# Optimization experiments

Hardware: AMD Instinct MI355X
Metric: run time of the kernel (lower is better)

## Reference

```python
import jax, jax.numpy as jnp
import numpy as np

B, L, D = 4, 2048, 2048
H, KVH = 16, 4
HD = D // H            # 128
G = H // KVH           # GQA group size
K_SEL = L // 4         # top_k_ratio = 0.25 -> 512
MAX_SEQ = 8192
THETA = 10000.0
SCALE = HD ** -0.5
NEG = -1e9


def _rope_tables(dim, max_len, theta):
    inv = 1.0 / theta ** (jnp.arange(0, dim, 2, dtype=jnp.float32) / dim)  # (dim/2,)
    ang = jnp.arange(max_len, dtype=jnp.float32)[:, None] * inv[None, :]   # (max_len, dim/2)
    return jnp.cos(ang), jnp.sin(ang)


def _apply_rope_pos(x, cos, sin, pos):
    # x: (B, h, K, HD), pos: (B, K) int positions
    c = cos[pos][:, None]  # (B,1,K,HD/2)
    s = sin[pos][:, None]
    x1, x2 = jnp.split(x, 2, axis=-1)
    return jnp.concatenate([x1 * c - x2 * s, x1 * s + x2 * c], axis=-1)


def setup_inputs() -> dict:
    key = jax.random.key(0)
    ks = jax.random.split(key, 8)
    std = 0.02
    x   = jax.random.normal(ks[0], (B, L, D), dtype=jnp.float32)
    Wq  = jax.random.normal(ks[1], (D, D), dtype=jnp.float32) * std
    Wkv = jax.random.normal(ks[2], (D, 2 * KVH * HD), dtype=jnp.float32) * std
    Wo  = jax.random.normal(ks[3], (D, D), dtype=jnp.float32) * std
    W1  = jax.random.normal(ks[4], (D, D // 4), dtype=jnp.float32) * std
    b1  = jnp.zeros((D // 4,), dtype=jnp.float32)
    W2  = jax.random.normal(ks[5], (D // 4, 1), dtype=jnp.float32) * std
    b2  = jnp.zeros((1,), dtype=jnp.float32)
    return {"x": x, "Wq": Wq, "Wkv": Wkv, "Wo": Wo,
            "W1": W1, "b1": b1, "W2": W2, "b2": b2}


def reference(x, Wq, Wkv, Wo, W1, b1, W2, b2):
    Bx, Lx, Dx = x.shape
    # 1. learned per-token importance scores
    imp = (jax.nn.gelu(x @ W1 + b1, approximate=False) @ W2 + b2)[..., 0]  # (B,L)
    # 2. top-k token selection, sorted to keep original order
    _, idx = jax.lax.top_k(imp, K_SEL)
    idx = jnp.sort(idx, axis=-1)                                           # (B,K)
    x_sel = jnp.take_along_axis(x, idx[..., None], axis=1)                 # (B,K,D)
    # 3. fused KV projection on the selected subset (GQA)
    kv = x_sel @ Wkv
    k, v = jnp.split(kv, 2, axis=-1)
    k = k.reshape(Bx, K_SEL, KVH, HD).transpose(0, 2, 1, 3)                # (B,KVH,K,HD)
    v = v.reshape(Bx, K_SEL, KVH, HD).transpose(0, 2, 1, 3)
    # 4. RoPE with original positions for K, contiguous positions for Q
    cos, sin = _rope_tables(HD, MAX_SEQ, THETA)
    k = _apply_rope_pos(k, cos, sin, idx)
    q = (x @ Wq).reshape(Bx, Lx, H, HD).transpose(0, 2, 1, 3)              # (B,H,L,HD)
    qpos = jnp.broadcast_to(jnp.arange(Lx)[None, :], (Bx, Lx))
    q = _apply_rope_pos(q, cos, sin, qpos)
    # 5. GQA head expansion + attention over gathered keys
    k = jnp.repeat(k, G, axis=1)                                           # (B,H,K,HD)
    v = jnp.repeat(v, G, axis=1)
    scores = jnp.einsum('bhld,bhkd->bhlk', q, k) * SCALE                   # (B,H,L,K)
    # causal mask on original key positions
    causal = idx[:, None, None, :] > jnp.arange(Lx)[None, None, :, None]
    scores = jnp.where(causal, NEG, scores)
    attn = jax.nn.softmax(scores, axis=-1)
    # 6. importance soft gating (gradient path into the scorer)
    gate = jax.nn.sigmoid(jnp.take_along_axis(imp, idx, axis=1))           # (B,K)
    attn = attn * gate[:, None, None, :]
    out = jnp.einsum('bhlk,bhkd->bhld', attn, v)                           # (B,H,L,HD)
    out = out.transpose(0, 2, 1, 3).reshape(Bx, Lx, Dx)
    return out @ Wo
```

## Files before the change

### kernel.cpp

```cpp
#include <hip/hip_runtime.h>
#include <math.h>

typedef unsigned short u16;
typedef __attribute__((ext_vector_type(8))) short short8;
typedef __attribute__((ext_vector_type(4))) float f32x4;

__device__ __forceinline__ float bf2f(u16 u) {
  return __uint_as_float(((unsigned)u) << 16);
}
__device__ __forceinline__ u16 f2bf(float f) {
  unsigned u = __float_as_uint(f);
  return (u16)((u + 0x7fffu + ((u >> 16) & 1u)) >> 16);
}

__device__ __forceinline__ void gload_lds16(const u16* g, u16* l) {
  __builtin_amdgcn_global_load_lds((const __attribute__((address_space(1))) unsigned int*)g,
                                   (__attribute__((address_space(3))) unsigned int*)l, 16, 0, 0);
}

__device__ __forceinline__ void stage_tile(const u16* __restrict__ gbase, int ldg,
                                           u16* lds, int w, int lane) {
  #pragma unroll
  for (int i = 0; i < 4; ++i) {
    int c = w * 4 + i;
    const u16* g = gbase + (size_t)(c * 8 + (lane >> 3)) * ldg + (lane & 7) * 8;
    gload_lds16(g, lds + c * 512);
  }
}

__global__ __launch_bounds__(256) void cvt_x_kernel(const float* __restrict__ x,
                                                    u16* __restrict__ xb,
                                                    u16* __restrict__ xlo) {
  size_t base = ((size_t)blockIdx.x * 256 + threadIdx.x) * 8;
  short8 hi, lo;
  #pragma unroll
  for (int i = 0; i < 8; ++i) {
    float v = x[base + i];
    u16 h = f2bf(v);
    hi[i] = (short)h;
    lo[i] = (short)f2bf(v - bf2f(h));
  }
  *(short8*)&xb[base] = hi;
  *(short8*)&xlo[base] = lo;
}

template <bool HILO>
__global__ __launch_bounds__(256) void transpose_cvt(const float* __restrict__ in,
                                                     u16* __restrict__ outH,
                                                     u16* __restrict__ outL,
                                                     int R, int C) {
  __shared__ u16 tH[64][72];
  __shared__ u16 tL[64][72];
  int rb = blockIdx.y * 64, cb = blockIdx.x * 64;
  int t = threadIdx.x;
  #pragma unroll
  for (int i = 0; i < 16; ++i) {
    int r = i * 4 + (t >> 6), c = t & 63;
    float v = in[(size_t)(rb + r) * C + cb + c];
    u16 h = f2bf(v);
    tH[r][c] = h;
    if (HILO) tL[r][c] = f2bf(v - bf2f(h));
  }
  __syncthreads();
  #pragma unroll
  for (int i = 0; i < 16; ++i) {
    int r = i * 4 + (t >> 6), c = t & 63;
    outH[(size_t)(cb + r) * R + rb + c] = tH[c][r];
    if (HILO) outL[(size_t)(cb + r) * R + rb + c] = tL[c][r];
  }
}

__global__ void ropetab_kernel(float* __restrict__ cosT, float* __restrict__ sinT) {
  int pos = blockIdx.x, i = threadIdx.x;
  float e = (float)(2 * i) * (1.0f / 128.0f);
  float inv = powf(10000.0f, -e);
  float ang = (float)pos * inv;
  cosT[pos * 64 + i] = cosf(ang);
  sinT[pos * 64 + i] = sinf(ang);
}

template <bool BF16OUT>
__global__ __launch_bounds__(512, 2) void gemm256(const u16* __restrict__ A,
                                                  const u16* __restrict__ BT,
                                                  float* __restrict__ Cf,
                                                  u16* __restrict__ Cb,
                                                  int M, int N, int K) {
  __shared__ __align__(1024) u16 smem[65536];
  const int bm = blockIdx.x * 256, bn = blockIdx.y * 256;
  const int t = threadIdx.x, lane = t & 63, w = t >> 6;
  const int ll = lane & 15, lh = lane >> 4;
  const int wr = w >> 2, wc = w & 3;
  const int NT = K >> 6;

  const int tt0 = t, tt1 = t + 512;
  const int r0 = tt0 >> 2, r1 = tt1 >> 2;
  const int c0 = (((tt0 & 3) ^ ((tt0 >> 3) & 3)) << 3);
  const int c1 = (((tt1 & 3) ^ ((tt1 >> 3) & 3)) << 3);
  const size_t aoff0 = (size_t)(bm + r0) * K + c0;
  const size_t aoff1 = (size_t)(bm + r1) * K + c1;
  const size_t boff0 = (size_t)(bn + r0) * K + c0;
  const size_t boff1 = (size_t)(bn + r1) * K + c1;

  const int swz = ((lh ^ ((ll >> 1) & 3)) << 3);
  const int arow = (wr * 128 + ll) * 32 + swz;
  const int brow = (wc * 64 + ll) * 32 + swz;

  f32x4 acc[8][4];
  #pragma unroll
  for (int mi = 0; mi < 8; ++mi)
    #pragma unroll
    for (int ni = 0; ni < 4; ++ni) acc[mi][ni] = f32x4{0.f, 0.f, 0.f, 0.f};

  short8 aq[8], bq[2];

#define G_STAGE(base, o0, o1, lds) \
  gload_lds16((base) + (o0), (lds) + w * 512); \
  gload_lds16((base) + (o1), (lds) + 4096 + w * 512)
#define RD_A(Sa, ks) \
  _Pragma("unroll") for (int mi = 0; mi < 8; ++mi) aq[mi] = *(const short8*)&(Sa)[(ks)*8192 + arow + mi * 512]
#define RD_B(Sb, ks, nh) \
  _Pragma("unroll") for (int n2 = 0; n2 < 2; ++n2) bq[n2] = *(const short8*)&(Sb)[(ks)*8192 + brow + ((nh)*2 + n2) * 512]
#define DO_MFMA(nh) \
  __builtin_amdgcn_s_setprio(1); \
  _Pragma("unroll") for (int mi = 0; mi < 8; ++mi) \
    _Pragma("unroll") for (int n2 = 0; n2 < 2; ++n2) \
      acc[mi][(nh)*2 + n2] = __builtin_amdgcn_mfma_f32_16x16x32_bf16(aq[mi], bq[n2], acc[mi][(nh)*2 + n2], 0, 0, 0); \
  __builtin_amdgcn_s_setprio(0)
#define VMW(n) asm volatile("s_waitcnt vmcnt(" #n ")" ::: "memory")

  G_STAGE(A, aoff0, aoff1, smem);
  G_STAGE(BT, boff0, boff1, smem + 16384);
  G_STAGE(A, aoff0 + 32, aoff1 + 32, smem + 8192);
  G_STAGE(BT, boff0 + 32, boff1 + 32, smem + 16384 + 8192);

  for (int kt = 0; kt < NT - 1; ++kt) {
    const int cur = kt & 1;
    u16* Sa = smem + cur * 32768;
    u16* Sb = Sa + 16384;
    u16* Pa = smem + (cur ^ 1) * 32768;
    u16* Pb = Pa + 16384;
    const size_t kg = (size_t)(kt + 1) * 64;
    VMW(4);
    __builtin_amdgcn_s_barrier();
    G_STAGE(A, aoff0 + kg, aoff1 + kg, Pa);
    RD_A(Sa, 0);
    RD_B(Sb, 0, 0);
    DO_MFMA(0);
    __builtin_amdgcn_s_barrier();
    G_STAGE(BT, boff0 + kg, boff1 + kg, Pb);
    RD_B(Sb, 0, 1);
    DO_MFMA(1);
    VMW(4);
    __builtin_amdgcn_s_barrier();
    G_STAGE(A, aoff0 + kg + 32, aoff1 + kg + 32, Pa + 8192);
    RD_A(Sa, 1);
    RD_B(Sb, 1, 0);
    DO_MFMA(0);
    __builtin_amdgcn_s_barrier();
    G_STAGE(BT, boff0 + kg + 32, boff1 + kg + 32, Pb + 8192);
    RD_B(Sb, 1, 1);
    DO_MFMA(1);
  }
  {
    const int cur = (NT - 1) & 1;
    u16* Sa = smem + cur * 32768;
    u16* Sb = Sa + 16384;
    VMW(4);
    __builtin_amdgcn_s_barrier();
    RD_A(Sa, 0); RD_B(Sb, 0, 0); DO_MFMA(0);
    __builtin_amdgcn_s_barrier();
    RD_B(Sb, 0, 1); DO_MFMA(1);
    VMW(0);
    __builtin_amdgcn_s_barrier();
    RD_A(Sa, 1); RD_B(Sb, 1, 0); DO_MFMA(0);
    __builtin_amdgcn_s_barrier();
    RD_B(Sb, 1, 1); DO_MFMA(1);
  }

  #pragma unroll
  for (int mi = 0; mi < 8; ++mi)
    #pragma unroll
    for (int ni = 0; ni < 4; ++ni)
      #pragma unroll
      for (int r = 0; r < 4; ++r) {
        int row = bm + wr * 128 + mi * 16 + lh * 4 + r;
        int col = bn + wc * 64 + ni * 16 + ll;
        float v = acc[mi][ni][r];
        if (BF16OUT) Cb[(size_t)row * N + col] = f2bf(v);
        else Cf[(size_t)row * N + col] = v;
      }
#undef G_STAGE
#undef RD_A
#undef RD_B
#undef DO_MFMA
#undef VMW
}

__global__ __launch_bounds__(256) void gemm_bt_gather(const u16* __restrict__ A,
                                                      const u16* __restrict__ BT,
                                                      const int* __restrict__ rowidx,
                                                      float* __restrict__ Cpart,
                                                      int M, int N, int K) {
  constexpr int BK = 64;
  __shared__ u16 As[128][BK + 8];
  __shared__ u16 Bs[128][BK + 8];
  const int bm = blockIdx.x * 128, bn = blockIdx.y * 128;
  const int kz = blockIdx.z;
  const int t = threadIdx.x, lane = t & 63, w = t >> 6;
  const int lh = lane >> 4, ll = lane & 15;
  const int wm = (w >> 1) * 64, wn = (w & 1) * 64;
  f32x4 acc[4][4];
  #pragma unroll
  for (int mt = 0; mt < 4; ++mt)
    #pragma unroll
    for (int nt = 0; nt < 4; ++nt) acc[mt][nt] = f32x4{0.f, 0.f, 0.f, 0.f};

  const int k0 = kz * (K / 2), k1 = k0 + K / 2;
  for (int kb = k0; kb < k1; kb += BK) {
    __syncthreads();
    #pragma unroll
    for (int i = 0; i < 4; ++i) {
      int e = t + i * 256;
      int row = e >> 3, c8 = e & 7;
      int arow = rowidx[bm + row];
      *(short8*)&As[row][c8 * 8] = *(const short8*)&A[(size_t)arow * K + kb + c8 * 8];
      *(short8*)&Bs[row][c8 * 8] = *(const short8*)&BT[(size_t)(bn + row) * K + kb + c8 * 8];
    }
    __syncthreads();
    #pragma unroll
    for (int ks = 0; ks < 2; ++ks) {
      short8 a[4], b[4];
      #pragma unroll
      for (int mt = 0; mt < 4; ++mt) a[mt] = *(const short8*)&As[wm + mt * 16 + ll][ks * 32 + lh * 8];
      #pragma unroll
      for (int nt = 0; nt < 4; ++nt) b[nt] = *(const short8*)&Bs[wn + nt * 16 + ll][ks * 32 + lh * 8];
      #pragma unroll
      for (int mt = 0; mt < 4; ++mt)
        #pragma unroll
        for (int nt = 0; nt < 4; ++nt)
          acc[mt][nt] = __builtin_amdgcn_mfma_f32_16x16x32_bf16(a[mt], b[nt], acc[mt][nt], 0, 0, 0);
    }
  }
  float* C = Cpart + (size_t)kz * M * N;
  #pragma unroll
  for (int mt = 0; mt < 4; ++mt)
    #pragma unroll
    for (int nt = 0; nt < 4; ++nt)
      #pragma unroll
      for (int r = 0; r < 4; ++r) {
        int row = bm + wm + mt * 16 + lh * 4 + r;
        int col = bn + wn + nt * 16 + ll;
        C[(size_t)row * N + col] = acc[mt][nt][r];
      }
}

__global__ __launch_bounds__(512) void gemm_scorer(const u16* __restrict__ Ahi,
                                                   const u16* __restrict__ Alo,
                                                   const u16* __restrict__ Bhi,
                                                   const u16* __restrict__ Blo,
                                                   float* __restrict__ Cpart,
                                                   int M, int N, int K) {
  __shared__ __align__(1024) u16 smem[49152];
  const int bm = blockIdx.x * 256, bn = blockIdx.y * 128;
  const int kz = blockIdx.z;
  const int t = threadIdx.x, lane = t & 63, w = t >> 6;
  const int ll = lane & 15, lh = lane >> 4;
  const int wr = w >> 2, wc = w & 3;

  const int cA0 = (w * 2) * 64 + lane;
  const int cA1 = (w * 2 + 1) * 64 + lane;
  const int cB = w * 64 + lane;
  const size_t offA0 = (size_t)(bm + (cA0 >> 2)) * K + (((cA0 & 3) ^ ((cA0 >> 3) & 3)) << 3);
  const size_t offA1 = (size_t)(bm + (cA1 >> 2)) * K + (((cA1 & 3) ^ ((cA1 >> 3) & 3)) << 3);
  const size_t offB = (size_t)(bn + (cB >> 2)) * K + (((cB & 3) ^ ((cB >> 3) & 3)) << 3);

  const int arow = wr * 128 + ll;
  const int brow = wc * 32 + ll;

  f32x4 acc[8][2];
  #pragma unroll
  for (int mi = 0; mi < 8; ++mi)
    #pragma unroll
    for (int ni = 0; ni < 2; ++ni) acc[mi][ni] = f32x4{0.f, 0.f, 0.f, 0.f};

#define S_STAGE(buf, kb) \
  gload_lds16(Ahi + offA0 + (kb), (buf) + cA0 * 8); \
  gload_lds16(Ahi + offA1 + (kb), (buf) + cA1 * 8); \
  gload_lds16(Alo + offA0 + (kb), (buf) + 8192 + cA0 * 8); \
  gload_lds16(Alo + offA1 + (kb), (buf) + 8192 + cA1 * 8); \
  gload_lds16(Bhi + offB + (kb), (buf) + 16384 + cB * 8); \
  gload_lds16(Blo + offB + (kb), (buf) + 20480 + cB * 8)
#define SVMW(n) asm volatile("s_waitcnt vmcnt(" #n ")" ::: "memory")

  const int k0 = kz * (K / 2);
  const int NT = (K / 2) / 32;

  S_STAGE(smem, k0);

  for (int kt = 0; kt < NT; ++kt) {
    const int cur = kt & 1;
    u16* S = smem + cur * 24576;
    SVMW(0);
    __builtin_amdgcn_s_barrier();
    if (kt + 1 < NT) { S_STAGE(smem + (cur ^ 1) * 24576, k0 + (kt + 1) * 32); }

    short8 aH[8], aL[8], bH[2], bL[2];
    #pragma unroll
    for (int mi = 0; mi < 8; ++mi) {
      int r = arow + mi * 16;
      int o = r * 32 + ((lh ^ ((r >> 1) & 3)) << 3);
      aH[mi] = *(const short8*)&S[o];
      aL[mi] = *(const short8*)&S[8192 + o];
    }
    #pragma unroll
    for (int ni = 0; ni < 2; ++ni) {
      int r = brow + ni * 16;
      int o = r * 32 + ((lh ^ ((r >> 1) & 3)) << 3);
      bH[ni] = *(const short8*)&S[16384 + o];
      bL[ni] = *(const short8*)&S[20480 + o];
    }
    __builtin_amdgcn_s_setprio(1);
    #pragma unroll
    for (int mi = 0; mi < 8; ++mi)
      #pragma unroll
      for (int ni = 0; ni < 2; ++ni)
        acc[mi][ni] = __builtin_amdgcn_mfma_f32_16x16x32_bf16(aH[mi], bH[ni], acc[mi][ni], 0, 0, 0);
    __builtin_amdgcn_s_setprio(0);
    __builtin_amdgcn_s_setprio(1);
    #pragma unroll
    for (int mi = 0; mi < 8; ++mi)
      #pragma unroll
      for (int ni = 0; ni < 2; ++ni)
        acc[mi][ni] = __builtin_amdgcn_mfma_f32_16x16x32_bf16(aH[mi], bL[ni], acc[mi][ni], 0, 0, 0);
    __builtin_amdgcn_s_setprio(0);
    __builtin_amdgcn_s_setprio(1);
    #pragma unroll
    for (int mi = 0; mi < 8; ++mi)
      #pragma unroll
      for (int ni = 0; ni < 2; ++ni)
        acc[mi][ni] = __builtin_amdgcn_mfma_f32_16x16x32_bf16(aL[mi], bH[ni], acc[mi][ni], 0, 0, 0);
    __builtin_amdgcn_s_setprio(0);
    __builtin_amdgcn_s_barrier();
  }

  float* C = Cpart + (size_t)kz * M * N;
  #pragma unroll
  for (int mi = 0; mi < 8; ++mi)
    #pragma unroll
    for (int ni = 0; ni < 2; ++ni)
      #pragma unroll
      for (int r = 0; r < 4; ++r) {
        int row = bm + wr * 128 + mi * 16 + lh * 4 + r;
        int col = bn + wc * 32 + ni * 16 + ll;
        C[(size_t)row * N + col] = acc[mi][ni][r];
      }
#undef S_STAGE
#undef SVMW
}

__global__ __launch_bounds__(256) void scorer_finish(const float* __restrict__ hg,
                                                     const float* __restrict__ b1,
                                                     const float* __restrict__ W2,
                                                     const float* __restrict__ b2,
                                                     float* __restrict__ imp) {
  int tok = blockIdx.x * 4 + (threadIdx.x >> 6);
  int lane = threadIdx.x & 63;
  const float* h0 = hg + (size_t)tok * 512;
  const float* h1 = hg + (size_t)8192 * 512 + (size_t)tok * 512;
  float s = 0.f;
  #pragma unroll
  for (int i = 0; i < 8; ++i) {
    int c = lane + i * 64;
    float v = h0[c] + h1[c] + b1[c];
    v = 0.5f * v * (1.0f + erff(v * 0.70710678118654752f));
    s += v * W2[c];
  }
  #pragma unroll
  for (int off = 32; off; off >>= 1) s += __shfl_xor(s, off, 64);
  if (lane == 0) imp[tok] = s + b2[0];
}

__global__ __launch_bounds__(1024) void topk_kernel(const float* __restrict__ imp,
                                                    int* __restrict__ idx_sel,
                                                    int* __restrict__ sel_rows,
                                                    float* __restrict__ gatev) {
  __shared__ float v[2048];
  __shared__ int ix[2048];
  __shared__ int ids[512];
  int b = blockIdx.x, t = threadIdx.x;
  for (int i = t; i < 2048; i += 1024) { v[i] = imp[b * 2048 + i]; ix[i] = i; }
  __syncthreads();
  for (int k = 2; k <= 2048; k <<= 1)
    for (int j = k >> 1; j > 0; j >>= 1) {
      int i = ((t & ~(j - 1)) << 1) | (t & (j - 1));
      int l2 = i | j;
      bool dir = ((i & k) == 0);
      float vi = v[i], vl = v[l2];
      int xi = ix[i], xl = ix[l2];
      bool g = (vi < vl) || (vi == vl && xi > xl);
      if (g == dir) { v[i] = vl; v[l2] = vi; ix[i] = xl; ix[l2] = xi; }
      __syncthreads();
    }
  if (t < 512) ids[t] = ix[t];
  __syncthreads();
  for (int k = 2; k <= 512; k <<= 1)
    for (int j = k >> 1; j > 0; j >>= 1) {
      if (t < 256) {
        int i = ((t & ~(j - 1)) << 1) | (t & (j - 1));
        int l2 = i | j;
        bool dir = ((i & k) == 0);
        int ai = ids[i], al = ids[l2];
        if ((ai > al) == dir) { ids[i] = al; ids[l2] = ai; }
      }
      __syncthreads();
    }
  if (t < 512) {
    int id = ids[t];
    idx_sel[b * 512 + t] = id;
    sel_rows[b * 512 + t] = b * 2048 + id;
    float g = imp[b * 2048 + id];
    gatev[b * 512 + t] = 1.0f / (1.0f + __expf(-g));
  }
}

__global__ __launch_bounds__(256) void rope_k2(const float* __restrict__ part,
                                               const int* __restrict__ idx_sel,
                                               const float* __restrict__ cosT,
                                               const float* __restrict__ sinT,
                                               u16* __restrict__ Kb) {
  int gid = blockIdx.x * 256 + threadIdx.x;
  int i = gid & 63;
  int s = (gid >> 6) & 511;
  int kvh = (gid >> 15) & 3;
  int b = gid >> 17;
  size_t src = (size_t)(b * 512 + s) * 1024 + kvh * 128 + i;
  float k1 = part[src] + part[src + 2097152];
  float k2 = part[src + 64] + part[src + 64 + 2097152];
  int pos = idx_sel[b * 512 + s];
  float c = cosT[pos * 64 + i], sn = sinT[pos * 64 + i];
  size_t dst = (size_t)((b * 4 + kvh) * 512 + s) * 128 + i;
  Kb[dst] = f2bf(k1 * c - k2 * sn);
  Kb[dst + 64] = f2bf(k1 * sn + k2 * c);
}

__global__ __launch_bounds__(256) void vtrans2(const float* __restrict__ part,
                                               const float* __restrict__ gatev,
                                               u16* __restrict__ VT) {
  int gid = blockIdx.x * 256 + threadIdx.x;
  int s = gid & 511;
  int d = (gid >> 9) & 127;
  int kvh = (gid >> 16) & 3;
  int b = gid >> 18;
  size_t src = (size_t)(b * 512 + s) * 1024 + 512 + kvh * 128 + d;
  float v = part[src] + part[src + 2097152];
  VT[(size_t)((b * 4 + kvh) * 128 + d) * 512 + s] = f2bf(v * gatev[b * 512 + s]);
}

__global__ __launch_bounds__(512) void attn_kernel(const u16* __restrict__ Qb,
                                                   const u16* __restrict__ Kb,
                                                   const u16* __restrict__ VTb,
                                                   const int* __restrict__ idxp,
                                                   const float* __restrict__ cosT,
                                                   const float* __restrict__ sinT,
                                                   u16* __restrict__ Ob) {
  __shared__ u16 Ks[64][132];
  __shared__ u16 Vs[128][76];
  __shared__ u16 Ps[8][16][68];
  __shared__ int idx_s[64];

  const int qt = (blockIdx.x + 4 * blockIdx.z) & 15;
  const int h = blockIdx.y, b = blockIdx.z;
  const int kvh = h >> 2;
  const int t = threadIdx.x, lane = t & 63, w = t >> 6;
  const int lh = lane >> 4, ll = lane & 15;
  const int q0 = qt * 128;
  const float SCALE_LOG2E = 0.12753102331f;

  int NT = 8;
  if (idxp[b * 512] <= q0) {
    NT = 1;
    while (NT < 8 && idxp[b * 512 + NT * 64] <= q0 + 127) ++NT;
  }

  const int lrow = q0 + w * 16 + ll;
  short8 aq[4];
  #pragma unroll
  for (int ks = 0; ks < 4; ++ks)
    aq[ks] = *(const short8*)&Qb[(size_t)(b * 2048 + lrow) * 2048 + h * 128 + ks * 32 + lh * 8];
  {
    const float* cp = cosT + (size_t)lrow * 64 + lh * 8;
    const float* sp = sinT + (size_t)lrow * 64 + lh * 8;
    short8 n0, n1, n2, n3;
    #pragma unroll
    for (int j = 0; j < 8; ++j) {
      float cA = cp[j], sA = sp[j], cB = cp[32 + j], sB = sp[32 + j];
      float x0 = bf2f((u16)aq[0][j]), x2 = bf2f((u16)aq[2][j]);
      float x1 = bf2f((u16)aq[1][j]), x3 = bf2f((u16)aq[3][j]);
      n0[j] = (short)f2bf(x0 * cA - x2 * sA);
      n2[j] = (short)f2bf(x0 * sA + x2 * cA);
      n1[j] = (short)f2bf(x1 * cB - x3 * sB);
      n3[j] = (short)f2bf(x1 * sB + x3 * cB);
    }
    aq[0] = n0; aq[1] = n1; aq[2] = n2; aq[3] = n3;
  }

  float m[4], lden[4];
  f32x4 O[8];
  #pragma unroll
  for (int r = 0; r < 4; ++r) { m[r] = -INFINITY; lden[r] = 0.f; }
  #pragma unroll
  for (int dt = 0; dt < 8; ++dt) O[dt] = f32x4{0.f, 0.f, 0.f, 0.f};

  for (int kt = 0; kt < NT; ++kt) {
    const int tmax = idxp[b * 512 + kt * 64 + 63];
    const bool nomask = (tmax <= q0 + w * 16);

    __syncthreads();
    #pragma unroll
    for (int i = 0; i < 2; ++i) {
      int e = t + i * 512;
      int krow = e >> 4, kc8 = e & 15;
      *(short8*)&Ks[krow][kc8 * 8] =
          *(const short8*)&Kb[(size_t)((b * 4 + kvh) * 512 + kt * 64 + krow) * 128 + kc8 * 8];
      int vrow = e >> 3, vc8 = e & 7;
      *(short8*)&Vs[vrow][vc8 * 8] =
          *(const short8*)&VTb[(size_t)((b * 4 + kvh) * 128 + vrow) * 512 + kt * 64 + vc8 * 8];
    }
    if (t < 64) idx_s[t] = idxp[b * 512 + kt * 64 + t];
    __syncthreads();

    f32x4 S[4];
    #pragma unroll
    for (int nt = 0; nt < 4; ++nt) S[nt] = f32x4{0.f, 0.f, 0.f, 0.f};
    #pragma unroll
    for (int nt = 0; nt < 4; ++nt)
      #pragma unroll
      for (int ks = 0; ks < 4; ++ks) {
        short8 bk = *(const short8*)&Ks[nt * 16 + ll][ks * 32 + lh * 8];
        S[nt] = __builtin_amdgcn_mfma_f32_16x16x32_bf16(aq[ks], bk, S[nt], 0, 0, 0);
      }

    float p[4][4], lmax[4];
    #pragma unroll
    for (int r = 0; r < 4; ++r) lmax[r] = -INFINITY;
    if (nomask) {
      #pragma unroll
      for (int nt = 0; nt < 4; ++nt)
        #pragma unroll
        for (int r = 0; r < 4; ++r) {
          float s = S[nt][r] * SCALE_LOG2E;
          p[nt][r] = s;
          lmax[r] = fmaxf(lmax[r], s);
        }
    } else {
      #pragma unroll
      for (int nt = 0; nt < 4; ++nt) {
        int kpos = idx_s[nt * 16 + ll];
        #pragma unroll
        for (int r = 0; r < 4; ++r) {
          int row = q0 + w * 16 + lh * 4 + r;
          float s = S[nt][r] * SCALE_LOG2E;
          if (kpos > row) s = -1e9f;
          p[nt][r] = s;
          lmax[r] = fmaxf(lmax[r], s);
        }
      }
    }
    #pragma unroll
    for (int off = 8; off; off >>= 1)
      #pragma unroll
      for (int r = 0; r < 4; ++r) lmax[r] = fmaxf(lmax[r], __shfl_xor(lmax[r], off, 64));

    bool need = false;
    #pragma unroll
    for (int r = 0; r < 4; ++r) need = need || (lmax[r] > m[r] + 8.0f);
    if (__any(need)) {
      #pragma unroll
      for (int r = 0; r < 4; ++r) {
        float mnew = fmaxf(m[r], lmax[r]);
        float alpha = exp2f(m[r] - mnew);
        m[r] = mnew;
        lden[r] *= alpha;
        #pragma unroll
        for (int dt = 0; dt < 8; ++dt) O[dt][r] *= alpha;
      }
    }

    float rs[4] = {0.f, 0.f, 0.f, 0.f};
    #pragma unroll
    for (int nt = 0; nt < 4; ++nt)
      #pragma unroll
      for (int r = 0; r < 4; ++r) {
        float e = exp2f(p[nt][r] - m[r]);
        p[nt][r] = e;
        rs[r] += e;
      }
    #pragma unroll
    for (int off = 8; off; off >>= 1)
      #pragma unroll
      for (int r = 0; r < 4; ++r) rs[r] += __shfl_xor(rs[r], off, 64);
    #pragma unroll
    for (int r = 0; r < 4; ++r) lden[r] += rs[r];

    #pragma unroll
    for (int nt = 0; nt < 4; ++nt)
      #pragma unroll
      for (int r = 0; r < 4; r += 2) {
        unsigned pk;
        asm("v_cvt_pk_bf16_f32 %0, %1, %2" : "=v"(pk) : "v"(p[nt][r]), "v"(p[nt][r + 1]));
        Ps[w][lh * 4 + r][nt * 16 + ll] = (u16)pk;
        Ps[w][lh * 4 + r + 1][nt * 16 + ll] = (u16)(pk >> 16);
      }
    #pragma unroll
    for (int ks = 0; ks < 2; ++ks) {
      short8 pa = *(const short8*)&Ps[w][ll][ks * 32 + lh * 8];
      #pragma unroll
      for (int dt = 0; dt < 8; ++dt) {
        short8 vb = *(const short8*)&Vs[dt * 16 + ll][ks * 32 + lh * 8];
        O[dt] = __builtin_amdgcn_mfma_f32_16x16x32_bf16(pa, vb, O[dt], 0, 0, 0);
      }
    }
  }

  #pragma unroll
  for (int dt = 0; dt < 8; ++dt)
    #pragma unroll
    for (int r = 0; r < 4; ++r) {
      int row = q0 + w * 16 + lh * 4 + r;
      int col = h * 128 + dt * 16 + ll;
      Ob[(size_t)(b * 2048 + row) * 2048 + col] = f2bf(O[dt][r] / lden[r]);
    }
}

extern "C" void kernel_launch(void* const* d_in, const int* in_sizes, int n_in,
                              void* d_out, int out_size, void* d_ws, size_t ws_size,
                              hipStream_t stream) {
  const float* x = (const float*)d_in[0];
  const float* Wq = (const float*)d_in[1];
  const float* Wkv = (const float*)d_in[2];
  const float* Wo = (const float*)d_in[3];
  const float* W1 = (const float*)d_in[4];
  const float* b1 = (const float*)d_in[5];
  const float* W2 = (const float*)d_in[6];
  const float* b2 = (const float*)d_in[7];
  float* out = (float*)d_out;

  char* ws = (char*)d_ws;
  size_t off = 0;
  auto alloc = [&](size_t bytes) {
    char* p = ws + off;
    off = (off + bytes + 255) & ~(size_t)255;
    return p;
  };
  u16* xb = (u16*)alloc((size_t)8192 * 2048 * 2);
  u16* xlo = (u16*)alloc((size_t)8192 * 2048 * 2);
  u16* W1Th = (u16*)alloc((size_t)512 * 2048 * 2);
  u16* W1Tl = (u16*)alloc((size_t)512 * 2048 * 2);
  u16* WqT = (u16*)alloc((size_t)2048 * 2048 * 2);
  u16* WkvT = (u16*)alloc((size_t)1024 * 2048 * 2);
  u16* WoT = (u16*)alloc((size_t)2048 * 2048 * 2);
  float* cosT = (float*)alloc((size_t)2048 * 64 * 4);
  float* sinT = (float*)alloc((size_t)2048 * 64 * 4);
  float* hg = (float*)alloc((size_t)2 * 8192 * 512 * 4);
  float* impv = (float*)alloc((size_t)8192 * 4);
  int* idx_sel = (int*)alloc((size_t)2048 * 4);
  int* sel_rows = (int*)alloc((size_t)2048 * 4);
  float* gatev = (float*)alloc((size_t)2048 * 4);
  u16* qbuf = (u16*)alloc((size_t)8192 * 2048 * 2);
  u16* Kbuf = (u16*)alloc((size_t)4 * 4 * 512 * 128 * 2);
  u16* VTbuf = (u16*)alloc((size_t)4 * 4 * 128 * 512 * 2);
  u16* attn_out = xlo;
  float* kvpart = hg;

  cvt_x_kernel<<<8192, 256, 0, stream>>>(x, xb, xlo);
  transpose_cvt<true><<<dim3(512 / 64, 2048 / 64), 256, 0, stream>>>(W1, W1Th, W1Tl, 2048, 512);
  transpose_cvt<false><<<dim3(32, 32), 256, 0, stream>>>(Wq, WqT, nullptr, 2048, 2048);
  transpose_cvt<false><<<dim3(16, 32), 256, 0, stream>>>(Wkv, WkvT, nullptr, 2048, 1024);
  transpose_cvt<false><<<dim3(32, 32), 256, 0, stream>>>(Wo, WoT, nullptr, 2048, 2048);
  ropetab_kernel<<<2048, 64, 0, stream>>>(cosT, sinT);

  gemm_scorer<<<dim3(32, 4, 2), 512, 0, stream>>>(xb, xlo, W1Th, W1Tl, hg, 8192, 512, 2048);
  scorer_finish<<<2048, 256, 0, stream>>>(hg, b1, W2, b2, impv);
  topk_kernel<<<4, 1024, 0, stream>>>(impv, idx_sel, sel_rows, gatev);

  gemm256<true><<<dim3(32, 8), 512, 0, stream>>>(xb, WqT, nullptr, qbuf, 8192, 2048, 2048);

  gemm_bt_gather<<<dim3(16, 8, 2), 256, 0, stream>>>(xb, WkvT, sel_rows, kvpart, 2048, 1024, 2048);
  rope_k2<<<2048, 256, 0, stream>>>(kvpart, idx_sel, cosT, sinT, Kbuf);
  vtrans2<<<4096, 256, 0, stream>>>(kvpart, gatev, VTbuf);

  attn_kernel<<<dim3(16, 16, 4), 512, 0, stream>>>(qbuf, Kbuf, VTbuf, idx_sel, cosT, sinT, attn_out);

  gemm256<false><<<dim3(32, 8), 512, 0, stream>>>(attn_out, WoT, out, nullptr, 8192, 2048, 2048);
}
```

Baseline: 382.3 us.

## Triple-buffer scorer GEMM loads and merge K/V finishing kernels

The scorer GEMM's LDS staging goes from double to triple buffering. Loads are issued two k-steps ahead, and the wait only requires the older stage (vmcnt 6), so more global-to-LDS latency is hidden. This raises LDS use from 96KB to 144KB per block, which can lower occupancy. Separately, the RoPE-K and V-transpose finishing kernels are merged into one launch to save a kernel launch.

```diff
diff --git a/kernel.cpp b/kernel.cpp
--- a/kernel.cpp
+++ b/kernel.cpp
@@ -16,16 +16,6 @@
 __device__ __forceinline__ void gload_lds16(const u16* g, u16* l) {
   __builtin_amdgcn_global_load_lds((const __attribute__((address_space(1))) unsigned int*)g,
                                    (__attribute__((address_space(3))) unsigned int*)l, 16, 0, 0);
-}
-
-__device__ __forceinline__ void stage_tile(const u16* __restrict__ gbase, int ldg,
-                                           u16* lds, int w, int lane) {
-  #pragma unroll
-  for (int i = 0; i < 4; ++i) {
-    int c = w * 4 + i;
-    const u16* g = gbase + (size_t)(c * 8 + (lane >> 3)) * ldg + (lane & 7) * 8;
-    gload_lds16(g, lds + c * 512);
-  }
 }
 
 __global__ __launch_bounds__(256) void cvt_x_kernel(const float* __restrict__ x,
@@ -260,7 +250,7 @@
                                                    const u16* __restrict__ Blo,
                                                    float* __restrict__ Cpart,
                                                    int M, int N, int K) {
-  __shared__ __align__(1024) u16 smem[49152];
+  __shared__ __align__(1024) u16 smem[73728];
   const int bm = blockIdx.x * 256, bn = blockIdx.y * 128;
   const int kz = blockIdx.z;
   const int t = threadIdx.x, lane = t & 63, w = t >> 6;
@@ -296,13 +286,13 @@
   const int NT = (K / 2) / 32;
 
   S_STAGE(smem, k0);
+  S_STAGE(smem + 24576, k0 + 32);
 
   for (int kt = 0; kt < NT; ++kt) {
-    const int cur = kt & 1;
-    u16* S = smem + cur * 24576;
-    SVMW(0);
-    __builtin_amdgcn_s_barrier();
-    if (kt + 1 < NT) { S_STAGE(smem + (cur ^ 1) * 24576, k0 + (kt + 1) * 32); }
+    u16* S = smem + (kt % 3) * 24576;
+    if (kt + 1 < NT) { SVMW(6); } else { SVMW(0); }
+    __builtin_amdgcn_s_barrier();
+    if (kt + 2 < NT) { S_STAGE(smem + ((kt + 2) % 3) * 24576, k0 + (kt + 2) * 32); }
 
     short8 aH[8], aL[8], bH[2], bL[2];
     #pragma unroll
@@ -423,37 +413,37 @@
   }
 }
 
-__global__ __launch_bounds__(256) void rope_k2(const float* __restrict__ part,
-                                               const int* __restrict__ idx_sel,
-                                               const float* __restrict__ cosT,
-                                               const float* __restrict__ sinT,
-                                               u16* __restrict__ Kb) {
+__global__ __launch_bounds__(256) void kv_finish(const float* __restrict__ part,
+                                                 const int* __restrict__ idx_sel,
+                                                 const float* __restrict__ cosT,
+                                                 const float* __restrict__ sinT,
+                                                 const float* __restrict__ gatev,
+                                                 u16* __restrict__ Kb,
+                                                 u16* __restrict__ VT) {
   int gid = blockIdx.x * 256 + threadIdx.x;
-  int i = gid & 63;
-  int s = (gid >> 6) & 511;
-  int kvh = (gid >> 15) & 3;
-  int b = gid >> 17;
-  size_t src = (size_t)(b * 512 + s) * 1024 + kvh * 128 + i;
-  float k1 = part[src] + part[src + 2097152];
-  float k2 = part[src + 64] + part[src + 64 + 2097152];
-  int pos = idx_sel[b * 512 + s];
-  float c = cosT[pos * 64 + i], sn = sinT[pos * 64 + i];
-  size_t dst = (size_t)((b * 4 + kvh) * 512 + s) * 128 + i;
-  Kb[dst] = f2bf(k1 * c - k2 * sn);
-  Kb[dst + 64] = f2bf(k1 * sn + k2 * c);
-}
-
-__global__ __launch_bounds__(256) void vtrans2(const float* __restrict__ part,
-                                               const float* __restrict__ gatev,
-                                               u16* __restrict__ VT) {
-  int gid = blockIdx.x * 256 + threadIdx.x;
-  int s = gid & 511;
-  int d = (gid >> 9) & 127;
-  int kvh = (gid >> 16) & 3;
-  int b = gid >> 18;
-  size_t src = (size_t)(b * 512 + s) * 1024 + 512 + kvh * 128 + d;
-  float v = part[src] + part[src + 2097152];
-  VT[(size_t)((b * 4 + kvh) * 128 + d) * 512 + s] = f2bf(v * gatev[b * 512 + s]);
+  if (gid < (1 << 19)) {
+    int i = gid & 63;
+    int s = (gid >> 6) & 511;
+    int kvh = (gid >> 15) & 3;
+    int b = gid >> 17;
+    size_t src = (size_t)(b * 512 + s) * 1024 + kvh * 128 + i;
+    float k1 = part[src] + part[src + 2097152];
+    float k2 = part[src + 64] + part[src + 64 + 2097152];
+    int pos = idx_sel[b * 512 + s];
+    float c = cosT[pos * 64 + i], sn = sinT[pos * 64 + i];
+    size_t dst = (size_t)((b * 4 + kvh) * 512 + s) * 128 + i;
+    Kb[dst] = f2bf(k1 * c - k2 * sn);
+    Kb[dst + 64] = f2bf(k1 * sn + k2 * c);
+  } else {
+    int g2 = gid - (1 << 19);
+    int s = g2 & 511;
+    int d = (g2 >> 9) & 127;
+    int kvh = (g2 >> 16) & 3;
+    int b = g2 >> 18;
+    size_t src = (size_t)(b * 512 + s) * 1024 + 512 + kvh * 128 + d;
+    float v = part[src] + part[src + 2097152];
+    VT[(size_t)((b * 4 + kvh) * 128 + d) * 512 + s] = f2bf(v * gatev[b * 512 + s]);
+  }
 }
 
 __global__ __launch_bounds__(512) void attn_kernel(const u16* __restrict__ Qb,
@@ -686,8 +676,7 @@
   gemm256<true><<<dim3(32, 8), 512, 0, stream>>>(xb, WqT, nullptr, qbuf, 8192, 2048, 2048);
 
   gemm_bt_gather<<<dim3(16, 8, 2), 256, 0, stream>>>(xb, WkvT, sel_rows, kvpart, 2048, 1024, 2048);
-  rope_k2<<<2048, 256, 0, stream>>>(kvpart, idx_sel, cosT, sinT, Kbuf);
-  vtrans2<<<4096, 256, 0, stream>>>(kvpart, gatev, VTbuf);
+  kv_finish<<<6144, 256, 0, stream>>>(kvpart, idx_sel, cosT, sinT, gatev, Kbuf, VTbuf);
 
   attn_kernel<<<dim3(16, 16, 4), 512, 0, stream>>>(qbuf, Kbuf, VTbuf, idx_sel, cosT, sinT, attn_out);
 
```

New measurement: 386.6 us. No clear change (+1.1%).
